# Performance work log

Measured on AMD Instinct MI355X. Metric: run time of the kernel, lower is better.

The kernel has to match this reference:

```python
import jax, jax.numpy as jnp
import numpy as np

QUERY_DIM = 256
HIDDEN_DIM = 256
NUM_HEADS = 8
HEAD_DIM = HIDDEN_DIM // NUM_HEADS
NORM_FACT = float(HIDDEN_DIM / NUM_HEADS) ** (-0.5)


def setup_inputs() -> dict:
    key = jax.random.key(0)
    ks = jax.random.split(key, 7)
    b, Q, H, W = 4, 300, 100, 100
    q = jax.random.normal(ks[0], (b, Q, QUERY_DIM), dtype=jnp.float32)
    k = jax.random.normal(ks[1], (b, QUERY_DIM, H, W), dtype=jnp.float32)
    mask = jax.random.randint(ks[2], (b, H, W), 0, 2).astype(jnp.bool_)
    # xavier_uniform for Linear(query_dim, hidden_dim): bound = sqrt(6/(fan_in+fan_out))
    bound = float(np.sqrt(6.0 / (QUERY_DIM + HIDDEN_DIM)))
    q_w = jax.random.uniform(ks[3], (HIDDEN_DIM, QUERY_DIM), jnp.float32, -bound, bound)
    k_w = jax.random.uniform(ks[4], (HIDDEN_DIM, QUERY_DIM), jnp.float32, -bound, bound)
    q_b = jnp.zeros((HIDDEN_DIM,), jnp.float32)
    k_b = jnp.zeros((HIDDEN_DIM,), jnp.float32)
    return {"q": q, "k": k, "mask": mask, "q_w": q_w, "q_b": q_b, "k_w": k_w, "k_b": k_b}


def reference(q, k, mask, q_w, q_b, k_w, k_b):
    b, Q, _ = q.shape
    _, C, H, W = k.shape
    # q_linear: [b,Q,query_dim] -> [b,Q,hidden]
    qp = jnp.einsum('bqc,hc->bqh', q, q_w) + q_b
    # k projection: 1x1 conv == channel-wise linear: [b,C,H,W] -> [b,hidden,H,W]
    kp = jnp.einsum('bchw,oc->bohw', k, k_w) + k_b[None, :, None, None]
    qh = qp.reshape(b, Q, NUM_HEADS, HEAD_DIM)
    kh = kp.reshape(b, NUM_HEADS, HEAD_DIM, H, W)
    # attention scores: [b, Q, n_heads, H, W]
    weights = jnp.einsum('bqnc,bnchw->bqnhw', qh * NORM_FACT, kh)
    if mask is not None:
        weights = jnp.where(mask[:, None, None, :, :], -jnp.inf, weights)
    # softmax over flattened (heads, H, W) — faithful to flatten(2) in the original
    flat = weights.reshape(b, Q, NUM_HEADS * H * W)
    weights = jax.nn.softmax(flat, axis=-1).reshape(b, Q, NUM_HEADS, H, W)
    return weights
```

## Files before the change

kernel.cpp:

```cpp
#include <hip/hip_runtime.h>
#include <math.h>

#define BB 4
#define QQ 300
#define CC 256
#define NH 8
#define HD 32
#define HWN 10000
#define NT 625
#define SCHUNK 125
#define STPC 5
#define OCHUNK 25
#define OTPC 25
#define QCH 4
#define NQT 5
#define MT 19
#define NORM_FACT 0.17677669529663687f

typedef __attribute__((ext_vector_type(8))) short short8_t;
typedef __attribute__((ext_vector_type(4))) float f32x4_t;
typedef __attribute__((ext_vector_type(4))) int   i32x4_t;

union FragU { uint32_t u[4]; short8_t v; };

__device__ __forceinline__ unsigned short bf16_rn(float x) {
    uint32_t u = __float_as_uint(x);
    return (unsigned short)((u + 0x7fffu + ((u >> 16) & 1u)) >> 16);
}
__device__ __forceinline__ float bf16_f(unsigned short h) {
    return __uint_as_float(((uint32_t)h) << 16);
}

__global__ void prep_kwB_kernel(const float* __restrict__ kw,
                                unsigned short* __restrict__ kwB_hi,
                                unsigned short* __restrict__ kwB_lo) {
    const int ot = blockIdx.x, ks = blockIdx.y;
    const int l = threadIdx.x;
    const int o = ot * 16 + (l & 15);
    const int c0 = ks * 32 + (l >> 4) * 8;
    const size_t base = ((size_t)(ot * 8 + ks) * 64 + l) * 8;
    #pragma unroll
    for (int j = 0; j < 8; ++j) {
        const float x = kw[o * CC + c0 + j];
        const unsigned short h = bf16_rn(x);
        kwB_hi[base + j] = h;
        kwB_lo[base + j] = bf16_rn(x - bf16_f(h));
    }
}

__global__ __launch_bounds__(256)
void qproj_kernel(const float* __restrict__ qin,
                  const unsigned short* __restrict__ qwB_hi,
                  const unsigned short* __restrict__ qwB_lo,
                  const float* __restrict__ qb,
                  unsigned short* __restrict__ qp_il) {
    const int wid = threadIdx.x >> 6, l = threadIdx.x & 63;
    const int rt = blockIdx.x;
    const int ot4 = wid;
    const int jb = (l >> 4) * 8;
    const int col = l & 15;

    FragU a_hi[8], a_lo[8];
    const float* abase = qin + ((size_t)rt * 16 + col) * CC;
    #pragma unroll
    for (int ks = 0; ks < 8; ++ks) {
        #pragma unroll
        for (int tt = 0; tt < 4; ++tt) {
            const int c = ks * 32 + jb + 2 * tt;
            const float x0 = abase[c];
            const float x1 = abase[c + 1];
            const unsigned short h0 = bf16_rn(x0), h1 = bf16_rn(x1);
            const unsigned short g0 = bf16_rn(x0 - bf16_f(h0));
            const unsigned short g1 = bf16_rn(x1 - bf16_f(h1));
            a_hi[ks].u[tt] = (uint32_t)h0 | ((uint32_t)h1 << 16);
            a_lo[ks].u[tt] = (uint32_t)g0 | ((uint32_t)g1 << 16);
        }
    }

    #pragma unroll 1
    for (int t = 0; t < 4; ++t) {
        const int ot = ot4 * 4 + t;
        f32x4_t c = {0.f, 0.f, 0.f, 0.f};
        #pragma unroll
        for (int ks = 0; ks < 8; ++ks) {
            const size_t fb = ((size_t)(ot * 8 + ks) * 64 + l) * 8;
            const short8_t bh = *reinterpret_cast<const short8_t*>(qwB_hi + fb);
            const short8_t bl = *reinterpret_cast<const short8_t*>(qwB_lo + fb);
            c = __builtin_amdgcn_mfma_f32_16x16x32_bf16(a_hi[ks].v, bh, c, 0, 0, 0);
            c = __builtin_amdgcn_mfma_f32_16x16x32_bf16(a_hi[ks].v, bl, c, 0, 0, 0);
            c = __builtin_amdgcn_mfma_f32_16x16x32_bf16(a_lo[ks].v, bh, c, 0, 0, 0);
        }
        const int o = ot * 16 + col;
        const int n = o >> 5, osub = o & 31;
        const float bias = qb[o];
        #pragma unroll
        for (int r = 0; r < 4; ++r) {
            const int row = rt * 16 + (l >> 4) * 4 + r;
            const float v = (c[r] + bias) * NORM_FACT;
            const size_t base = ((size_t)row * NH + n) * 64 + osub;
            const unsigned short h = bf16_rn(v);
            qp_il[base]      = h;
            qp_il[base + 32] = bf16_rn(v - bf16_f(h));
        }
    }
}

__global__ __launch_bounds__(256)
void kproj_kernel(const float* __restrict__ kin,
                  const unsigned short* __restrict__ kwB_hi,
                  const unsigned short* __restrict__ kwB_lo,
                  const float* __restrict__ kb,
                  unsigned short* __restrict__ kp_il) {
    __shared__ float kf[CC][17];
    const int wid = threadIdx.x >> 6, l = threadIdx.x & 63;
    const int bu  = blockIdx.x;
    const int hwt = bu % NT;
    const int b   = bu / NT;
    const int ot4 = wid;

    {
        const int tid = threadIdx.x;
        const float* kb0 = kin + (size_t)b * CC * HWN + hwt * 16;
        #pragma unroll
        for (int iter = 0; iter < 4; ++iter) {
            const int c   = iter * 64 + (tid >> 2);
            const int cl  = (tid & 3) * 4;
            const float4 v = *reinterpret_cast<const float4*>(
                kb0 + (size_t)c * HWN + cl);
            kf[c][cl]     = v.x;
            kf[c][cl + 1] = v.y;
            kf[c][cl + 2] = v.z;
            kf[c][cl + 3] = v.w;
        }
    }
    __syncthreads();

    const int jb  = (l >> 4) * 8;
    const int col = l & 15;

    f32x4_t acc[4];
    #pragma unroll
    for (int t = 0; t < 4; ++t) {
        const float bias = kb[(ot4 * 4 + t) * 16 + col];
        acc[t] = {bias, bias, bias, bias};
    }

    #pragma unroll 2
    for (int ks = 0; ks < 8; ++ks) {
        FragU a_hi, a_lo;
        #pragma unroll
        for (int tt = 0; tt < 4; ++tt) {
            const int c = ks * 32 + jb + 2 * tt;
            const float x0 = kf[c][col];
            const float x1 = kf[c + 1][col];
            const unsigned short h0 = bf16_rn(x0), h1 = bf16_rn(x1);
            const unsigned short g0 = bf16_rn(x0 - bf16_f(h0));
            const unsigned short g1 = bf16_rn(x1 - bf16_f(h1));
            a_hi.u[tt] = (uint32_t)h0 | ((uint32_t)h1 << 16);
            a_lo.u[tt] = (uint32_t)g0 | ((uint32_t)g1 << 16);
        }
        #pragma unroll
        for (int t = 0; t < 4; ++t) {
            const int ot = ot4 * 4 + t;
            const size_t fb = ((size_t)(ot * 8 + ks) * 64 + l) * 8;
            const short8_t bh = *reinterpret_cast<const short8_t*>(kwB_hi + fb);
            const short8_t bl = *reinterpret_cast<const short8_t*>(kwB_lo + fb);
            acc[t] = __builtin_amdgcn_mfma_f32_16x16x32_bf16(a_hi.v, bh, acc[t], 0, 0, 0);
            acc[t] = __builtin_amdgcn_mfma_f32_16x16x32_bf16(a_hi.v, bl, acc[t], 0, 0, 0);
            acc[t] = __builtin_amdgcn_mfma_f32_16x16x32_bf16(a_lo.v, bh, acc[t], 0, 0, 0);
        }
    }

    #pragma unroll
    for (int t = 0; t < 4; ++t) {
        const int o = (ot4 * 4 + t) * 16 + col;
        const int n = o >> 5, osub = o & 31;
        #pragma unroll
        for (int r = 0; r < 4; ++r) {
            const int hwrow = hwt * 16 + (l >> 4) * 4 + r;
            const size_t base = ((size_t)(b * HWN + hwrow) * NH + n) * 64 + osub;
            const float v = acc[t][r];
            const unsigned short h = bf16_rn(v);
            kp_il[base]      = h;
            kp_il[base + 32] = bf16_rn(v - bf16_f(h));
        }
    }
}

__global__ __launch_bounds__(256)
void attn_stats_kernel(const unsigned short* __restrict__ qp_il,
                       const unsigned short* __restrict__ kp_il,
                       const int* __restrict__ mask,
                       float* __restrict__ partials) {
    const int wid = threadIdx.x >> 6, l = threadIdx.x & 63;
    const int wu = blockIdx.x * 4 + wid;
    const int qh = wu & 1;
    int tmp = wu >> 1;
    const int ch = tmp % SCHUNK; tmp /= SCHUNK;
    const int n = tmp & 7;
    const int b = tmp >> 3;

    short8_t ah[STPC], al[STPC];
    float mf[STPC][4];
    #pragma unroll
    for (int t = 0; t < STPC; ++t) {
        const int tile = ch * STPC + t;
        const int hwr = tile * 16 + (l & 15);
        const size_t abase = ((size_t)(b * HWN + hwr) * NH + n) * 64 + (l >> 4) * 8;
        ah[t] = *reinterpret_cast<const short8_t*>(kp_il + abase);
        al[t] = *reinterpret_cast<const short8_t*>(kp_il + abase + 32);
        const int hw4 = tile * 16 + (l >> 4) * 4;
        const i32x4_t mv = *reinterpret_cast<const i32x4_t*>(mask + b * HWN + hw4);
        mf[t][0] = mv.x ? 0.f : 1.f;
        mf[t][1] = mv.y ? 0.f : 1.f;
        mf[t][2] = mv.z ? 0.f : 1.f;
        mf[t][3] = mv.w ? 0.f : 1.f;
    }

    const int qt0 = qh * 10;
    const int qt1 = qh ? MT : 10;
    #pragma unroll 2
    for (int qt = qt0; qt < qt1; ++qt) {
        const int qa = qt * 16 + (l & 15);
        const int qcl = qa < QQ ? qa : QQ - 1;
        const size_t bbase = ((size_t)(b * QQ + qcl) * NH + n) * 64 + (l >> 4) * 8;
        const short8_t bh = *reinterpret_cast<const short8_t*>(qp_il + bbase);
        const short8_t bl = *reinterpret_cast<const short8_t*>(qp_il + bbase + 32);

        float a = 0.f;
        #pragma unroll
        for (int t = 0; t < STPC; ++t) {
            f32x4_t c = {0.f, 0.f, 0.f, 0.f};
            c = __builtin_amdgcn_mfma_f32_16x16x32_bf16(ah[t], bh, c, 0, 0, 0);
            c = __builtin_amdgcn_mfma_f32_16x16x32_bf16(ah[t], bl, c, 0, 0, 0);
            c = __builtin_amdgcn_mfma_f32_16x16x32_bf16(al[t], bh, c, 0, 0, 0);
            a += __expf(c[0]) * mf[t][0] + __expf(c[1]) * mf[t][1]
               + __expf(c[2]) * mf[t][2] + __expf(c[3]) * mf[t][3];
        }
        a += __shfl_xor(a, 16, 64);
        a += __shfl_xor(a, 32, 64);
        if (l < 16) {
            const int qr = qt * 16 + l;
            if (qr < QQ)
                partials[(((size_t)b * QQ + qr) * NH + n) * SCHUNK + ch] = a;
        }
    }
}

__global__ void invsum_kernel(const float* __restrict__ partials,
                              float* __restrict__ invS) {
    const int row = blockIdx.x;
    const int l = threadIdx.x;
    float s = 0.f;
    const float* p = partials + (size_t)row * (NH * SCHUNK);
    for (int i = l; i < NH * SCHUNK; i += 64) s += p[i];
    #pragma unroll
    for (int m = 1; m < 64; m <<= 1) s += __shfl_xor(s, m, 64);
    if (l == 0) invS[row] = 1.0f / s;
}

__global__ __launch_bounds__(256)
void attn_out_kernel(const unsigned short* __restrict__ qp_il,
                     const unsigned short* __restrict__ kp_il,
                     const int* __restrict__ mask,
                     const float* __restrict__ invS,
                     float* __restrict__ out) {
    const int wid = threadIdx.x >> 6, l = threadIdx.x & 63;
    const int wu = blockIdx.x * 4 + wid;
    const int ch = wu % OCHUNK;
    int tmp = wu / OCHUNK;
    const int qc = tmp % QCH; tmp /= QCH;
    const int n = tmp & 7;
    const int b = tmp >> 3;

    short8_t bh[NQT], bl[NQT];
    float isv[NQT];
    float* optr[NQT];
    bool qok[NQT];
    #pragma unroll
    for (int tt = 0; tt < NQT; ++tt) {
        const int qa = (qc * NQT + tt) * 16 + (l & 15);
        const int qcl = qa < QQ ? qa : QQ - 1;
        qok[tt] = qa < QQ;
        const size_t bbase = ((size_t)(b * QQ + qcl) * NH + n) * 64 + (l >> 4) * 8;
        bh[tt] = *reinterpret_cast<const short8_t*>(qp_il + bbase);
        bl[tt] = *reinterpret_cast<const short8_t*>(qp_il + bbase + 32);
        isv[tt] = invS[b * QQ + qcl];
        optr[tt] = out + (((size_t)b * QQ + qcl) * NH + n) * HWN;
    }

    #pragma unroll 2
    for (int t = 0; t < OTPC; ++t) {
        const int tile = ch * OTPC + t;
        const int hwr = tile * 16 + (l & 15);
        const size_t abase = ((size_t)(b * HWN + hwr) * NH + n) * 64 + (l >> 4) * 8;
        const short8_t ah = *reinterpret_cast<const short8_t*>(kp_il + abase);
        const short8_t al = *reinterpret_cast<const short8_t*>(kp_il + abase + 32);
        const int hw4 = tile * 16 + (l >> 4) * 4;
        const i32x4_t mv = *reinterpret_cast<const i32x4_t*>(mask + b * HWN + hw4);
        const float m0 = mv.x ? 0.f : 1.f, m1 = mv.y ? 0.f : 1.f;
        const float m2 = mv.z ? 0.f : 1.f, m3 = mv.w ? 0.f : 1.f;
        #pragma unroll
        for (int tt = 0; tt < NQT; ++tt) {
            f32x4_t c = {0.f, 0.f, 0.f, 0.f};
            c = __builtin_amdgcn_mfma_f32_16x16x32_bf16(ah, bh[tt], c, 0, 0, 0);
            c = __builtin_amdgcn_mfma_f32_16x16x32_bf16(ah, bl[tt], c, 0, 0, 0);
            c = __builtin_amdgcn_mfma_f32_16x16x32_bf16(al, bh[tt], c, 0, 0, 0);
            const float is = isv[tt];
            f32x4_t rv;
            rv[0] = __expf(c[0]) * is * m0;
            rv[1] = __expf(c[1]) * is * m1;
            rv[2] = __expf(c[2]) * is * m2;
            rv[3] = __expf(c[3]) * is * m3;
            if (qok[tt])
                __builtin_nontemporal_store(rv,
                    reinterpret_cast<f32x4_t*>(optr[tt] + hw4));
        }
    }
}

extern "C" void kernel_launch(void* const* d_in, const int* in_sizes, int n_in,
                              void* d_out, int out_size, void* d_ws, size_t ws_size,
                              hipStream_t stream) {
    const float* q    = (const float*)d_in[0];
    const float* k    = (const float*)d_in[1];
    const int*   mask = (const int*)d_in[2];
    const float* qw   = (const float*)d_in[3];
    const float* qb   = (const float*)d_in[4];
    const float* kw   = (const float*)d_in[5];
    const float* kb   = (const float*)d_in[6];
    float* out = (float*)d_out;

    char* wsb = (char*)d_ws;
    unsigned short* kp_il = (unsigned short*)wsb;
    unsigned short* qp_il = (unsigned short*)(wsb + 40960000);
    float* invS           = (float*)(wsb + 40960000 + 1228800);

    unsigned short* kwB_hi = (unsigned short*)d_out;
    unsigned short* kwB_lo = kwB_hi + 65536;
    unsigned short* qwB_hi = kwB_hi + 131072;
    unsigned short* qwB_lo = kwB_hi + 196608;
    float* partials = (float*)((char*)d_out + (4u << 20));

    prep_kwB_kernel<<<dim3(16, 8), 64, 0, stream>>>(kw, kwB_hi, kwB_lo);
    prep_kwB_kernel<<<dim3(16, 8), 64, 0, stream>>>(qw, qwB_hi, qwB_lo);
    qproj_kernel<<<75, 256, 0, stream>>>(q, qwB_hi, qwB_lo, qb, qp_il);
    kproj_kernel<<<BB * NT, 256, 0, stream>>>(k, kwB_hi, kwB_lo, kb, kp_il);
    attn_stats_kernel<<<(BB * NH * SCHUNK * 2) / 4, 256, 0, stream>>>(
        qp_il, kp_il, mask, partials);
    invsum_kernel<<<BB * QQ, 64, 0, stream>>>(partials, invS);
    attn_out_kernel<<<(BB * NH * QCH * OCHUNK) / 4, 256, 0, stream>>>(
        qp_il, kp_il, mask, invS, out);
}
```

Baseline: 243.1 us.

## Stage attention output tiles in LDS for coalesced row-contiguous stores

The output kernel is reorganized so each block handles one 16-query tile by 256 spatial positions for a single batch and head. Each wave computes four 16x16 MFMA tiles and writes the results into a shared-memory buffer. After a barrier, the block writes each query row as one contiguous 1KB segment. The goal is to replace the scattered 16-byte stores of the old per-wave layout with fully coalesced row writes to the large output. In exchange it adds a block barrier and LDS traffic, uses far more blocks, and reuses each query fragment much less per wave.

```diff
diff --git a/kernel.cpp b/kernel.cpp
--- a/kernel.cpp
+++ b/kernel.cpp
@@ -10,10 +10,7 @@
 #define NT 625
 #define SCHUNK 125
 #define STPC 5
-#define OCHUNK 25
-#define OTPC 25
-#define QCH 4
-#define NQT 5
+#define OCH 40
 #define MT 19
 #define NORM_FACT 0.17677669529663687f
 
@@ -265,33 +262,28 @@
                      const int* __restrict__ mask,
                      const float* __restrict__ invS,
                      float* __restrict__ out) {
+    __shared__ float obuf[16][260];
     const int wid = threadIdx.x >> 6, l = threadIdx.x & 63;
-    const int wu = blockIdx.x * 4 + wid;
-    const int ch = wu % OCHUNK;
-    int tmp = wu / OCHUNK;
-    const int qc = tmp % QCH; tmp /= QCH;
-    const int n = tmp & 7;
-    const int b = tmp >> 3;
-
-    short8_t bh[NQT], bl[NQT];
-    float isv[NQT];
-    float* optr[NQT];
-    bool qok[NQT];
-    #pragma unroll
-    for (int tt = 0; tt < NQT; ++tt) {
-        const int qa = (qc * NQT + tt) * 16 + (l & 15);
-        const int qcl = qa < QQ ? qa : QQ - 1;
-        qok[tt] = qa < QQ;
-        const size_t bbase = ((size_t)(b * QQ + qcl) * NH + n) * 64 + (l >> 4) * 8;
-        bh[tt] = *reinterpret_cast<const short8_t*>(qp_il + bbase);
-        bl[tt] = *reinterpret_cast<const short8_t*>(qp_il + bbase + 32);
-        isv[tt] = invS[b * QQ + qcl];
-        optr[tt] = out + (((size_t)b * QQ + qcl) * NH + n) * HWN;
-    }
-
-    #pragma unroll 2
-    for (int t = 0; t < OTPC; ++t) {
-        const int tile = ch * OTPC + t;
+    int wu = blockIdx.x;
+    const int qt = wu % MT; wu /= MT;
+    const int och = wu % OCH; wu /= OCH;
+    const int n = wu & 7;
+    const int b = wu >> 3;
+
+    const int qa = qt * 16 + (l & 15);
+    const int qcl = qa < QQ ? qa : QQ - 1;
+    const size_t bbase = ((size_t)(b * QQ + qcl) * NH + n) * 64 + (l >> 4) * 8;
+    const short8_t bh = *reinterpret_cast<const short8_t*>(qp_il + bbase);
+    const short8_t bl = *reinterpret_cast<const short8_t*>(qp_il + bbase + 32);
+    const float is = invS[b * QQ + qcl];
+
+    const int ntile = (och == OCH - 1) ? 1 : 16;
+
+    #pragma unroll
+    for (int tl = 0; tl < 4; ++tl) {
+        const int tloc = wid * 4 + tl;
+        if (tloc >= ntile) break;
+        const int tile = och * 16 + tloc;
         const int hwr = tile * 16 + (l & 15);
         const size_t abase = ((size_t)(b * HWN + hwr) * NH + n) * 64 + (l >> 4) * 8;
         const short8_t ah = *reinterpret_cast<const short8_t*>(kp_il + abase);
@@ -300,21 +292,31 @@
         const i32x4_t mv = *reinterpret_cast<const i32x4_t*>(mask + b * HWN + hw4);
         const float m0 = mv.x ? 0.f : 1.f, m1 = mv.y ? 0.f : 1.f;
         const float m2 = mv.z ? 0.f : 1.f, m3 = mv.w ? 0.f : 1.f;
-        #pragma unroll
-        for (int tt = 0; tt < NQT; ++tt) {
-            f32x4_t c = {0.f, 0.f, 0.f, 0.f};
-            c = __builtin_amdgcn_mfma_f32_16x16x32_bf16(ah, bh[tt], c, 0, 0, 0);
-            c = __builtin_amdgcn_mfma_f32_16x16x32_bf16(ah, bl[tt], c, 0, 0, 0);
-            c = __builtin_amdgcn_mfma_f32_16x16x32_bf16(al, bh[tt], c, 0, 0, 0);
-            const float is = isv[tt];
-            f32x4_t rv;
-            rv[0] = __expf(c[0]) * is * m0;
-            rv[1] = __expf(c[1]) * is * m1;
-            rv[2] = __expf(c[2]) * is * m2;
-            rv[3] = __expf(c[3]) * is * m3;
-            if (qok[tt])
-                __builtin_nontemporal_store(rv,
-                    reinterpret_cast<f32x4_t*>(optr[tt] + hw4));
+
+        f32x4_t c = {0.f, 0.f, 0.f, 0.f};
+        c = __builtin_amdgcn_mfma_f32_16x16x32_bf16(ah, bh, c, 0, 0, 0);
+        c = __builtin_amdgcn_mfma_f32_16x16x32_bf16(ah, bl, c, 0, 0, 0);
+        c = __builtin_amdgcn_mfma_f32_16x16x32_bf16(al, bh, c, 0, 0, 0);
+        f32x4_t rv;
+        rv[0] = __expf(c[0]) * is * m0;
+        rv[1] = __expf(c[1]) * is * m1;
+        rv[2] = __expf(c[2]) * is * m2;
+        rv[3] = __expf(c[3]) * is * m3;
+
+        const int col = tloc * 16 + ((l >> 4) << 2);
+        *reinterpret_cast<f32x4_t*>(&obuf[l & 15][col]) = rv;
+    }
+    __syncthreads();
+
+    const int nhw = ntile * 16;
+    #pragma unroll
+    for (int r = 0; r < 4; ++r) {
+        const int qi = wid * 4 + r;
+        const int qg = qt * 16 + qi;
+        if (qg < QQ && l * 4 < nhw) {
+            const f32x4_t v = *reinterpret_cast<const f32x4_t*>(&obuf[qi][l * 4]);
+            __builtin_nontemporal_store(v, reinterpret_cast<f32x4_t*>(
+                out + (((size_t)b * QQ + qg) * NH + n) * HWN + och * 256 + l * 4));
         }
     }
 }
@@ -349,6 +351,6 @@
     attn_stats_kernel<<<(BB * NH * SCHUNK * 2) / 4, 256, 0, stream>>>(
         qp_il, kp_il, mask, partials);
     invsum_kernel<<<BB * QQ, 64, 0, stream>>>(partials, invS);
-    attn_out_kernel<<<(BB * NH * QCH * OCHUNK) / 4, 256, 0, stream>>>(
+    attn_out_kernel<<<BB * NH * OCH * MT, 256, 0, stream>>>(
         qp_il, kp_il, mask, invS, out);
 }
```

Result: no change. 238.5 us (-1.9%).
